# Kernel tuning notes

Hardware: AMD Instinct MI355X
Metric: run time of the kernel (lower is better)

## Reference

```python
import jax, jax.numpy as jnp
import numpy as np

B, S, D, H = 2, 2048, 768, 12
HD = D // H


def setup_inputs() -> dict:
    key = jax.random.key(0)
    ks = jax.random.split(key, 8)
    scale = 1.0 / np.sqrt(D)
    inp = {
        "q": jax.random.normal(ks[0], (B, S, D), jnp.float32),
        "k": jax.random.normal(ks[1], (B, S, D), jnp.float32),
        "v": jax.random.normal(ks[2], (B, S, D), jnp.float32),
        # causal mask: 1.0 where attention is disallowed (upper triangle)
        "mask": jnp.triu(jnp.ones((S, S), jnp.float32), k=1)[None, None, :, :],
        "Wq": jax.random.normal(ks[3], (D, D), jnp.float32) * scale,
        "bq": jnp.zeros((D,), jnp.float32),
        "Wk": jax.random.normal(ks[4], (D, D), jnp.float32) * scale,
        "bk": jnp.zeros((D,), jnp.float32),
        "Wv": jax.random.normal(ks[5], (D, D), jnp.float32) * scale,
        "bv": jnp.zeros((D,), jnp.float32),
        "Wo": jax.random.normal(ks[6], (D, D), jnp.float32) * scale,
        "bo": jnp.zeros((D,), jnp.float32),
    }
    return inp


def _split_heads(x):
    # [B, S, D] -> [B, H, S, HD]
    b, s, _ = x.shape
    return x.reshape(b, s, H, HD).transpose(0, 2, 1, 3)


def reference(q, k, v, mask, Wq, bq, Wk, bk, Wv, bv, Wo, bo):
    qh = _split_heads(q @ Wq + bq)
    kh = _split_heads(k @ Wk + bk)
    vh = _split_heads(v @ Wv + bv)
    scale = 1.0 / jnp.sqrt(jnp.asarray(HD, qh.dtype))
    # [B, H, Sq, Sk] — full attention matrix, as in the original
    scores = jnp.einsum("bhqd,bhkd->bhqk", qh, kh) * scale
    scores = scores + mask * -1e9
    attn = jax.nn.softmax(scores, axis=-1)  # dropout is identity at inference
    out = jnp.einsum("bhqk,bhkd->bhqd", attn, vh)
    out = out.transpose(0, 2, 1, 3).reshape(q.shape[0], -1, D)
    return out @ Wo + bo
```

## Files before the change

kernel.cpp:

```cpp
#include <hip/hip_runtime.h>

#define SEQ    2048
#define NB     2
#define DMODEL 768
#define NH     12
#define HDIM   64
#define BS     (NB * SEQ)

typedef __bf16  bf16x8  __attribute__((ext_vector_type(8)));
typedef ushort  ushort8 __attribute__((ext_vector_type(8)));
typedef float   floatx4 __attribute__((ext_vector_type(4)));

#define GLOBAL_AS __attribute__((address_space(1)))
#define LDS_AS    __attribute__((address_space(3)))

union PackU8 { ushort u[8]; uint4 v; };
union PackU4 { ushort u[4]; uint2 v; };

__device__ __forceinline__ ushort f2bf(float x) {
    union { float f; unsigned u; } t; t.f = x;
    unsigned r = t.u + 0x7fffu + ((t.u >> 16) & 1u);
    return (ushort)(r >> 16);
}

__device__ __forceinline__ bf16x8 ld_frag(const ushort* p) {
    return __builtin_bit_cast(bf16x8, *(const ushort8*)p);
}

__global__ void convert_x(const float* __restrict__ q, const float* __restrict__ k,
                          const float* __restrict__ v,
                          ushort* __restrict__ qo, ushort* __restrict__ ko,
                          ushort* __restrict__ vo)
{
    const float* src = blockIdx.z == 0 ? q : blockIdx.z == 1 ? k : v;
    ushort*      dst = blockIdx.z == 0 ? qo : blockIdx.z == 1 ? ko : vo;
    const int i = (blockIdx.x * 256 + threadIdx.x) * 4;
    const float4 f = *(const float4*)(src + i);
    ushort4 o;
    o.x = f2bf(f.x); o.y = f2bf(f.y); o.z = f2bf(f.z); o.w = f2bf(f.w);
    *(ushort4*)(dst + i) = o;
}

__global__ __launch_bounds__(256)
void convert_wT(const float* __restrict__ wq, const float* __restrict__ wk,
                const float* __restrict__ wv, const float* __restrict__ wo,
                ushort* __restrict__ wtcat, ushort* __restrict__ wto)
{
    __shared__ float Tf[64][69];
    const int z = blockIdx.z;
    const float* w = z == 0 ? wq : z == 1 ? wk : z == 2 ? wv : wo;
    ushort*      o = z < 3 ? wtcat + (size_t)z * DMODEL * DMODEL : wto;
    const int k0 = blockIdx.x * 64, n0 = blockIdx.y * 64;
    const int tid = threadIdx.x;
#pragma unroll
    for (int p = 0; p < 4; ++p) {
        const int idx = tid + p * 256;
        const int r = idx >> 4, c = (idx & 15) * 4;
        const float4 f = *(const float4*)&w[(size_t)(k0 + r) * DMODEL + n0 + c];
        Tf[r][c] = f.x; Tf[r][c + 1] = f.y; Tf[r][c + 2] = f.z; Tf[r][c + 3] = f.w;
    }
    __syncthreads();
#pragma unroll
    for (int p = 0; p < 2; ++p) {
        const int idx = tid + p * 256;
        const int n = idx >> 3, kk = (idx & 7) * 8;
        PackU8 pk;
#pragma unroll
        for (int j = 0; j < 8; ++j) pk.u[j] = f2bf(Tf[kk + j][n]);
        *(uint4*)&o[(size_t)(n0 + n) * DMODEL + k0 + kk] = pk.v;
    }
}

__global__ __launch_bounds__(256)
void gemm_qkv(const ushort* __restrict__ xq, const ushort* __restrict__ xk,
              const ushort* __restrict__ xv, const ushort* __restrict__ WT,
              const float* __restrict__ bq, const float* __restrict__ bk,
              const float* __restrict__ bv,
              ushort* __restrict__ oq, ushort* __restrict__ ok,
              ushort* __restrict__ ov)
{
    __shared__ __align__(16) ushort As[128 * 32];
    __shared__ __align__(16) ushort Bs[128 * 32];

    const int z = blockIdx.y / 6;
    const ushort* X = z == 0 ? xq : z == 1 ? xk : xv;

    const int tid  = threadIdx.x;
    const int lane = tid & 63;
    const int w    = tid >> 6;
    const int l15  = lane & 15;
    const int quad = lane >> 4;
    const int wm   = (w >> 1) * 64;
    const int wn   = (w & 1) * 64;
    const int row0 = blockIdx.x * 128;
    const int col0 = blockIdx.y * 128;

    floatx4 acc[4][4];
    const floatx4 fzero = {0.f, 0.f, 0.f, 0.f};
#pragma unroll
    for (int i = 0; i < 4; ++i)
#pragma unroll
        for (int j = 0; j < 4; ++j) acc[i][j] = fzero;

    const int rin = lane >> 2;
    const int gc  = (lane & 3) * 8;

    for (int k0 = 0; k0 < DMODEL; k0 += 32) {
#pragma unroll
        for (int p = 0; p < 2; ++p) {
            const int ch = w * 2 + p;
            const int r  = ch * 16 + rin;
            __builtin_amdgcn_global_load_lds(
                (const GLOBAL_AS uint*)&X[(size_t)(row0 + r) * DMODEL + k0 + gc],
                (LDS_AS uint*)&As[ch * 512], 16, 0, 0);
            __builtin_amdgcn_global_load_lds(
                (const GLOBAL_AS uint*)&WT[(size_t)(col0 + r) * DMODEL + k0 + gc],
                (LDS_AS uint*)&Bs[ch * 512], 16, 0, 0);
        }
        __syncthreads();

        bf16x8 af[4], bfr[4];
#pragma unroll
        for (int t = 0; t < 4; ++t) {
            af[t]  = ld_frag(&As[(wm + t * 16 + l15) * 32 + quad * 8]);
            bfr[t] = ld_frag(&Bs[(wn + t * 16 + l15) * 32 + quad * 8]);
        }
#pragma unroll
        for (int ti = 0; ti < 4; ++ti)
#pragma unroll
            for (int tj = 0; tj < 4; ++tj)
                acc[ti][tj] = __builtin_amdgcn_mfma_f32_16x16x32_bf16(
                    af[ti], bfr[tj], acc[ti][tj], 0, 0, 0);
        __syncthreads();
    }

    const int c0 = (blockIdx.y % 6) * 128;
    const float*  bias = z == 0 ? bq : z == 1 ? bk : bv;
    ushort*       out  = z == 0 ? oq : z == 1 ? ok : ov;
    const float   sc   = (z == 0) ? 0.18033688f : 1.f;
#pragma unroll
    for (int tj = 0; tj < 4; ++tj) {
        const int c_l = c0 + wn + tj * 16 + l15;
        const float bb = bias[c_l];
        const int h  = c_l >> 6;
        const int dd = c_l & 63;
#pragma unroll
        for (int ti = 0; ti < 4; ++ti) {
#pragma unroll
            for (int ri = 0; ri < 4; ++ri) {
                const int r_g = row0 + wm + ti * 16 + quad * 4 + ri;
                const int b   = r_g >> 11;
                const int s   = r_g & (SEQ - 1);
                out[(((size_t)(b * NH + h) * SEQ + s) << 6) + dd] =
                    f2bf((acc[ti][tj][ri] + bb) * sc);
            }
        }
    }
}

__global__ __launch_bounds__(256)
void gemm_out(const ushort* __restrict__ X, const ushort* __restrict__ WT,
              const float* __restrict__ bias, float* __restrict__ fo)
{
    __shared__ __align__(16) ushort As[64][40];
    __shared__ __align__(16) ushort Bs[128][40];

    const int tid  = threadIdx.x;
    const int lane = tid & 63;
    const int wv   = tid >> 6;
    const int wm   = (wv >> 1) * 32;
    const int wn   = (wv & 1) * 64;
    const int l15  = lane & 15;
    const int quad = lane >> 4;
    const int row0 = blockIdx.x * 64;
    const int col0 = blockIdx.y * 128;

    floatx4 acc[2][4];
    const floatx4 fzero = {0.f, 0.f, 0.f, 0.f};
#pragma unroll
    for (int i = 0; i < 2; ++i)
#pragma unroll
        for (int j = 0; j < 4; ++j) acc[i][j] = fzero;

    const int sr = tid >> 2;
    const int sc = (tid & 3) * 8;

    for (int k0 = 0; k0 < DMODEL; k0 += 32) {
        *(uint4*)&As[sr][sc] = *(const uint4*)&X[(size_t)(row0 + sr) * DMODEL + k0 + sc];
#pragma unroll
        for (int p = 0; p < 2; ++p) {
            const int r = sr + p * 64;
            *(uint4*)&Bs[r][sc] = *(const uint4*)&WT[(size_t)(col0 + r) * DMODEL + k0 + sc];
        }
        __syncthreads();

        bf16x8 af[2], bfr[4];
#pragma unroll
        for (int t = 0; t < 2; ++t)
            af[t] = ld_frag(&As[wm + t * 16 + l15][quad * 8]);
#pragma unroll
        for (int t = 0; t < 4; ++t)
            bfr[t] = ld_frag(&Bs[wn + t * 16 + l15][quad * 8]);
#pragma unroll
        for (int ti = 0; ti < 2; ++ti)
#pragma unroll
            for (int tj = 0; tj < 4; ++tj)
                acc[ti][tj] = __builtin_amdgcn_mfma_f32_16x16x32_bf16(
                    af[ti], bfr[tj], acc[ti][tj], 0, 0, 0);
        __syncthreads();
    }

#pragma unroll
    for (int tj = 0; tj < 4; ++tj) {
        const int c_g = col0 + wn + tj * 16 + l15;
        const float bb = bias[c_g];
#pragma unroll
        for (int ti = 0; ti < 2; ++ti)
#pragma unroll
            for (int ri = 0; ri < 4; ++ri) {
                const int r_g = row0 + wm + ti * 16 + quad * 4 + ri;
                fo[(size_t)r_g * DMODEL + c_g] = acc[ti][tj][ri] + bb;
            }
    }
}

__global__ void transpose_v(const ushort* __restrict__ vh, ushort* __restrict__ vt)
{
    __shared__ __align__(16) ushort T[64][72];
    const int bh = blockIdx.y;
    const int s0 = blockIdx.x * 64;
    const ushort* src = vh + (size_t)bh * SEQ * HDIM;
    ushort*       dst = vt + (size_t)bh * HDIM * SEQ;

#pragma unroll
    for (int p = 0; p < 2; ++p) {
        const int idx = threadIdx.x + p * 256;
        const int r = idx >> 3, c = (idx & 7) * 8;
        *(uint4*)&T[r][c] = *(const uint4*)&src[(size_t)(s0 + r) * HDIM + c];
    }
    __syncthreads();
#pragma unroll
    for (int p = 0; p < 2; ++p) {
        const int idx = threadIdx.x + p * 256;
        const int d = idx >> 3, c = (idx & 7) * 8;
        PackU8 pk;
#pragma unroll
        for (int j = 0; j < 8; ++j) pk.u[j] = T[c + j][d];
        *(uint4*)&dst[(size_t)d * SEQ + s0 + c] = pk.v;
    }
}

__global__ __launch_bounds__(64)
void attn_mfma(const ushort* __restrict__ qh, const ushort* __restrict__ kh,
               const ushort* __restrict__ vt, ushort* __restrict__ ctx)
{
    __shared__ __align__(16) ushort Ps[32][64];

    const int lane = threadIdx.x;
    const int l15  = lane & 15;
    const int quad = lane >> 4;
    const int e3   = l15 & 7;

    const int id  = blockIdx.x;
    const int xcd = id & 7;
    const int jj  = id >> 3;
    const int g   = jj >> 6;
    const int qt  = 63 - (jj & 63);
    const int bh  = xcd + 8 * g;
    const int b   = bh / NH, h = bh - b * NH;
    const int nk  = (qt >> 1) + 1;
    const size_t base = (size_t)bh * SEQ * HDIM;

    bf16x8 qf0[2], qf1[2];
#pragma unroll
    for (int ks = 0; ks < 2; ++ks) {
        qf0[ks] = ld_frag(&qh[base + (size_t)(qt * 32 +      l15) * HDIM + ks * 32 + quad * 8]);
        qf1[ks] = ld_frag(&qh[base + (size_t)(qt * 32 + 16 + l15) * HDIM + ks * 32 + quad * 8]);
    }

    float l0 = 0.f, l1 = 0.f;
    floatx4 O[4][2];
    const floatx4 fzero = {0.f, 0.f, 0.f, 0.f};
#pragma unroll
    for (int dj = 0; dj < 4; ++dj) { O[dj][0] = fzero; O[dj][1] = fzero; }

    const int rg0 = qt * 32 + l15;

    auto load_k = [&](bf16x8 (&kf)[4][2], int t) {
        const int c0 = t * 64;
#pragma unroll
        for (int nj = 0; nj < 4; ++nj)
#pragma unroll
            for (int ks = 0; ks < 2; ++ks)
                kf[nj][ks] = ld_frag(
                    &kh[base + (size_t)(c0 + nj * 16 + l15) * HDIM + ks * 32 + quad * 8]);
    };

    auto body = [&](const bf16x8 (&kf)[4][2], int t) {
        const int  c0   = t * 64;
        const bool diag = (t == nk - 1);

        bf16x8 vf[4][2];
#pragma unroll
        for (int dj = 0; dj < 4; ++dj)
#pragma unroll
            for (int ks = 0; ks < 2; ++ks)
                vf[dj][ks] = ld_frag(
                    &vt[base + (size_t)(dj * 16 + l15) * SEQ + c0 + ks * 32 + quad * 8]);

        floatx4 S[4][2];
        __builtin_amdgcn_s_setprio(1);
#pragma unroll
        for (int nj = 0; nj < 4; ++nj) {
            S[nj][0] = __builtin_amdgcn_mfma_f32_16x16x32_bf16(kf[nj][0], qf0[0], fzero, 0, 0, 0);
            S[nj][1] = __builtin_amdgcn_mfma_f32_16x16x32_bf16(kf[nj][0], qf1[0], fzero, 0, 0, 0);
            S[nj][0] = __builtin_amdgcn_mfma_f32_16x16x32_bf16(kf[nj][1], qf0[1], S[nj][0], 0, 0, 0);
            S[nj][1] = __builtin_amdgcn_mfma_f32_16x16x32_bf16(kf[nj][1], qf1[1], S[nj][1], 0, 0, 0);
        }
        __builtin_amdgcn_s_setprio(0);

        float rs0 = 0.f, rs1 = 0.f;
#pragma unroll
        for (int nj = 0; nj < 4; ++nj) {
            PackU4 p0, p1;
#pragma unroll
            for (int ri = 0; ri < 4; ++ri) {
                const int krow = c0 + nj * 16 + quad * 4 + ri;
                float v0 = __builtin_amdgcn_exp2f(S[nj][0][ri]);
                float v1 = __builtin_amdgcn_exp2f(S[nj][1][ri]);
                if (diag) {
                    if (krow > rg0)      v0 = 0.f;
                    if (krow > rg0 + 16) v1 = 0.f;
                }
                rs0 += v0; rs1 += v1;
                union { float f; unsigned u; } t0, t1;
                t0.f = v0; t1.f = v1;
                p0.u[ri] = (ushort)(t0.u >> 16);
                p1.u[ri] = (ushort)(t1.u >> 16);
            }
            *(uint2*)&Ps[l15     ][(nj * 16 + quad * 4) ^ (e3 << 3)] = p0.v;
            *(uint2*)&Ps[16 + l15][(nj * 16 + quad * 4) ^ (e3 << 3)] = p1.v;
        }
        rs0 += __shfl_xor(rs0, 16); rs0 += __shfl_xor(rs0, 32);
        rs1 += __shfl_xor(rs1, 16); rs1 += __shfl_xor(rs1, 32);
        l0 += rs0; l1 += rs1;

        bf16x8 pf0[2], pf1[2];
#pragma unroll
        for (int ks = 0; ks < 2; ++ks) {
            pf0[ks] = ld_frag(&Ps[l15     ][(ks * 32 + quad * 8) ^ (e3 << 3)]);
            pf1[ks] = ld_frag(&Ps[16 + l15][(ks * 32 + quad * 8) ^ (e3 << 3)]);
        }

        __builtin_amdgcn_s_setprio(1);
#pragma unroll
        for (int dj = 0; dj < 4; ++dj)
#pragma unroll
            for (int ks = 0; ks < 2; ++ks) {
                O[dj][0] = __builtin_amdgcn_mfma_f32_16x16x32_bf16(pf0[ks], vf[dj][ks], O[dj][0], 0, 0, 0);
                O[dj][1] = __builtin_amdgcn_mfma_f32_16x16x32_bf16(pf1[ks], vf[dj][ks], O[dj][1], 0, 0, 0);
            }
        __builtin_amdgcn_s_setprio(0);
    };

    bf16x8 kfA[4][2], kfB[4][2];
    load_k(kfA, 0);
    int t = 0;
    for (; t + 1 < nk; t += 2) {
        load_k(kfB, t + 1);
        body(kfA, t);
        if (t + 2 < nk) load_k(kfA, t + 2);
        body(kfB, t + 1);
    }
    if (t < nk) body(kfA, t);

    const float i0 = 1.f / l0, i1 = 1.f / l1;
    float ib0[4], ib1[4];
#pragma unroll
    for (int ri = 0; ri < 4; ++ri) {
        ib0[ri] = __shfl(i0, quad * 4 + ri);
        ib1[ri] = __shfl(i1, quad * 4 + ri);
    }
#pragma unroll
    for (int dj = 0; dj < 4; ++dj)
#pragma unroll
        for (int ri = 0; ri < 4; ++ri) {
            const int r0 = qt * 32 + quad * 4 + ri;
            ctx[((size_t)b * SEQ + r0) * DMODEL + h * HDIM + dj * 16 + l15] =
                f2bf(O[dj][0][ri] * ib0[ri]);
            ctx[((size_t)b * SEQ + r0 + 16) * DMODEL + h * HDIM + dj * 16 + l15] =
                f2bf(O[dj][1][ri] * ib1[ri]);
        }
}

extern "C" void kernel_launch(void* const* d_in, const int* in_sizes, int n_in,
                              void* d_out, int out_size, void* d_ws, size_t ws_size,
                              hipStream_t stream)
{
    const float* q  = (const float*)d_in[0];
    const float* k  = (const float*)d_in[1];
    const float* v  = (const float*)d_in[2];
    const float* Wq = (const float*)d_in[4];
    const float* bq = (const float*)d_in[5];
    const float* Wk = (const float*)d_in[6];
    const float* bk = (const float*)d_in[7];
    const float* Wv = (const float*)d_in[8];
    const float* bv = (const float*)d_in[9];
    const float* Wo = (const float*)d_in[10];
    const float* bo = (const float*)d_in[11];
    float* out = (float*)d_out;

    char* ws = (char*)d_ws;
    const size_t ACT = (size_t)BS * DMODEL * 2;
    ushort* qx    = (ushort*)(ws);
    ushort* kx    = (ushort*)(ws + ACT);
    ushort* vx    = (ushort*)(ws + 2 * ACT);
    ushort* qhp   = (ushort*)(ws + 3 * ACT);
    ushort* khp   = (ushort*)(ws + 4 * ACT);
    ushort* vhp   = (ushort*)(ws + 5 * ACT);
    ushort* wtcat = (ushort*)(ws + 6 * ACT);
    ushort* wto   = wtcat + (size_t)3 * DMODEL * DMODEL;
    ushort* vhT   = vx;
    ushort* ctx   = qx;

    convert_x<<<dim3(BS * DMODEL / 1024, 1, 3), 256, 0, stream>>>(q, k, v, qx, kx, vx);
    convert_wT<<<dim3(12, 12, 4), 256, 0, stream>>>(Wq, Wk, Wv, Wo, wtcat, wto);
    gemm_qkv<<<dim3(BS / 128, 18), 256, 0, stream>>>(
        qx, kx, vx, wtcat, bq, bk, bv, qhp, khp, vhp);
    transpose_v<<<dim3(SEQ / 64, NB * NH), 256, 0, stream>>>(vhp, vhT);
    attn_mfma<<<dim3(1536), 64, 0, stream>>>(qhp, khp, vhT, ctx);
    gemm_out<<<dim3(BS / 64, DMODEL / 128), 256, 0, stream>>>(ctx, wto, bo, out);
}
```

Baseline: 213.2 us.

## Split attention KV loop across four waves per block with LDS exchange

Runs the attention kernel with four waves per query tile. Each wave computes QK^T and exp for a different 64-key tile and writes the probabilities to its own LDS slot. After a barrier, every wave multiplies all four P tiles against its own 16-column slice of V. Row sums are combined through LDS at the end. This shortens each block's serial KV chain and lowers per-wave register use, at the cost of two barriers per step, dropping the K double-buffering, and redundant P reads from LDS.

```diff
diff --git a/kernel.cpp b/kernel.cpp
--- a/kernel.cpp
+++ b/kernel.cpp
@@ -250,13 +250,16 @@
     }
 }
 
-__global__ __launch_bounds__(64)
+__global__ __launch_bounds__(256, 4)
 void attn_mfma(const ushort* __restrict__ qh, const ushort* __restrict__ kh,
                const ushort* __restrict__ vt, ushort* __restrict__ ctx)
 {
-    __shared__ __align__(16) ushort Ps[32][64];
-
-    const int lane = threadIdx.x;
+    __shared__ __align__(16) ushort Ps[4][32][64];
+    __shared__ __align__(16) float  Lred[4][2][16];
+
+    const int tid  = threadIdx.x;
+    const int lane = tid & 63;
+    const int wv   = tid >> 6;
     const int l15  = lane & 15;
     const int quad = lane >> 4;
     const int e3   = l15 & 7;
@@ -279,118 +282,105 @@
     }
 
     float l0 = 0.f, l1 = 0.f;
-    floatx4 O[4][2];
+    floatx4 O0, O1;
     const floatx4 fzero = {0.f, 0.f, 0.f, 0.f};
-#pragma unroll
-    for (int dj = 0; dj < 4; ++dj) { O[dj][0] = fzero; O[dj][1] = fzero; }
+    O0 = fzero; O1 = fzero;
 
     const int rg0 = qt * 32 + l15;
 
-    auto load_k = [&](bf16x8 (&kf)[4][2], int t) {
-        const int c0 = t * 64;
-#pragma unroll
-        for (int nj = 0; nj < 4; ++nj)
-#pragma unroll
-            for (int ks = 0; ks < 2; ++ks)
-                kf[nj][ks] = ld_frag(
-                    &kh[base + (size_t)(c0 + nj * 16 + l15) * HDIM + ks * 32 + quad * 8]);
-    };
-
-    auto body = [&](const bf16x8 (&kf)[4][2], int t) {
-        const int  c0   = t * 64;
-        const bool diag = (t == nk - 1);
-
-        bf16x8 vf[4][2];
-#pragma unroll
-        for (int dj = 0; dj < 4; ++dj)
-#pragma unroll
-            for (int ks = 0; ks < 2; ++ks)
-                vf[dj][ks] = ld_frag(
-                    &vt[base + (size_t)(dj * 16 + l15) * SEQ + c0 + ks * 32 + quad * 8]);
-
-        floatx4 S[4][2];
-        __builtin_amdgcn_s_setprio(1);
-#pragma unroll
-        for (int nj = 0; nj < 4; ++nj) {
-            S[nj][0] = __builtin_amdgcn_mfma_f32_16x16x32_bf16(kf[nj][0], qf0[0], fzero, 0, 0, 0);
-            S[nj][1] = __builtin_amdgcn_mfma_f32_16x16x32_bf16(kf[nj][0], qf1[0], fzero, 0, 0, 0);
-            S[nj][0] = __builtin_amdgcn_mfma_f32_16x16x32_bf16(kf[nj][1], qf0[1], S[nj][0], 0, 0, 0);
-            S[nj][1] = __builtin_amdgcn_mfma_f32_16x16x32_bf16(kf[nj][1], qf1[1], S[nj][1], 0, 0, 0);
-        }
-        __builtin_amdgcn_s_setprio(0);
-
-        float rs0 = 0.f, rs1 = 0.f;
-#pragma unroll
-        for (int nj = 0; nj < 4; ++nj) {
-            PackU4 p0, p1;
-#pragma unroll
-            for (int ri = 0; ri < 4; ++ri) {
-                const int krow = c0 + nj * 16 + quad * 4 + ri;
-                float v0 = __builtin_amdgcn_exp2f(S[nj][0][ri]);
-                float v1 = __builtin_amdgcn_exp2f(S[nj][1][ri]);
-                if (diag) {
-                    if (krow > rg0)      v0 = 0.f;
-                    if (krow > rg0 + 16) v1 = 0.f;
+    for (int t4 = 0; t4 < nk; t4 += 4) {
+        const int kt = t4 + wv;
+
+        if (kt < nk) {
+            const int  c0   = kt * 64;
+            const bool diag = (kt == nk - 1);
+
+            bf16x8 kf[4][2];
+#pragma unroll
+            for (int nj = 0; nj < 4; ++nj)
+#pragma unroll
+                for (int ks = 0; ks < 2; ++ks)
+                    kf[nj][ks] = ld_frag(
+                        &kh[base + (size_t)(c0 + nj * 16 + l15) * HDIM + ks * 32 + quad * 8]);
+
+            float rs0 = 0.f, rs1 = 0.f;
+#pragma unroll
+            for (int nj = 0; nj < 4; ++nj) {
+                floatx4 s0, s1;
+                s0 = __builtin_amdgcn_mfma_f32_16x16x32_bf16(kf[nj][0], qf0[0], fzero, 0, 0, 0);
+                s1 = __builtin_amdgcn_mfma_f32_16x16x32_bf16(kf[nj][0], qf1[0], fzero, 0, 0, 0);
+                s0 = __builtin_amdgcn_mfma_f32_16x16x32_bf16(kf[nj][1], qf0[1], s0, 0, 0, 0);
+                s1 = __builtin_amdgcn_mfma_f32_16x16x32_bf16(kf[nj][1], qf1[1], s1, 0, 0, 0);
+
+                PackU4 p0, p1;
+#pragma unroll
+                for (int ri = 0; ri < 4; ++ri) {
+                    const int krow = c0 + nj * 16 + quad * 4 + ri;
+                    float v0 = __builtin_amdgcn_exp2f(s0[ri]);
+                    float v1 = __builtin_amdgcn_exp2f(s1[ri]);
+                    if (diag) {
+                        if (krow > rg0)      v0 = 0.f;
+                        if (krow > rg0 + 16) v1 = 0.f;
+                    }
+                    rs0 += v0; rs1 += v1;
+                    union { float f; unsigned u; } t0u, t1u;
+                    t0u.f = v0; t1u.f = v1;
+                    p0.u[ri] = (ushort)(t0u.u >> 16);
+                    p1.u[ri] = (ushort)(t1u.u >> 16);
                 }
-                rs0 += v0; rs1 += v1;
-                union { float f; unsigned u; } t0, t1;
-                t0.f = v0; t1.f = v1;
-                p0.u[ri] = (ushort)(t0.u >> 16);
-                p1.u[ri] = (ushort)(t1.u >> 16);
+                *(uint2*)&Ps[wv][l15     ][(nj * 16 + quad * 4) ^ (e3 << 3)] = p0.v;
+                *(uint2*)&Ps[wv][16 + l15][(nj * 16 + quad * 4) ^ (e3 << 3)] = p1.v;
             }
-            *(uint2*)&Ps[l15     ][(nj * 16 + quad * 4) ^ (e3 << 3)] = p0.v;
-            *(uint2*)&Ps[16 + l15][(nj * 16 + quad * 4) ^ (e3 << 3)] = p1.v;
-        }
-        rs0 += __shfl_xor(rs0, 16); rs0 += __shfl_xor(rs0, 32);
-        rs1 += __shfl_xor(rs1, 16); rs1 += __shfl_xor(rs1, 32);
-        l0 += rs0; l1 += rs1;
-
-        bf16x8 pf0[2], pf1[2];
-#pragma unroll
-        for (int ks = 0; ks < 2; ++ks) {
-            pf0[ks] = ld_frag(&Ps[l15     ][(ks * 32 + quad * 8) ^ (e3 << 3)]);
-            pf1[ks] = ld_frag(&Ps[16 + l15][(ks * 32 + quad * 8) ^ (e3 << 3)]);
-        }
-
-        __builtin_amdgcn_s_setprio(1);
-#pragma unroll
-        for (int dj = 0; dj < 4; ++dj)
-#pragma unroll
-            for (int ks = 0; ks < 2; ++ks) {
-                O[dj][0] = __builtin_amdgcn_mfma_f32_16x16x32_bf16(pf0[ks], vf[dj][ks], O[dj][0], 0, 0, 0);
-                O[dj][1] = __builtin_amdgcn_mfma_f32_16x16x32_bf16(pf1[ks], vf[dj][ks], O[dj][1], 0, 0, 0);
+            rs0 += __shfl_xor(rs0, 16); rs0 += __shfl_xor(rs0, 32);
+            rs1 += __shfl_xor(rs1, 16); rs1 += __shfl_xor(rs1, 32);
+            l0 += rs0; l1 += rs1;
+        }
+        __syncthreads();
+
+        const int na = (nk - t4 < 4) ? (nk - t4) : 4;
+#pragma unroll
+        for (int w = 0; w < 4; ++w) {
+            if (w < na) {
+                const int c0w = (t4 + w) * 64;
+                bf16x8 vf[2], pf0[2], pf1[2];
+#pragma unroll
+                for (int ks = 0; ks < 2; ++ks) {
+                    vf[ks]  = ld_frag(&vt[base + (size_t)(wv * 16 + l15) * SEQ + c0w + ks * 32 + quad * 8]);
+                    pf0[ks] = ld_frag(&Ps[w][l15     ][(ks * 32 + quad * 8) ^ (e3 << 3)]);
+                    pf1[ks] = ld_frag(&Ps[w][16 + l15][(ks * 32 + quad * 8) ^ (e3 << 3)]);
+                }
+#pragma unroll
+                for (int ks = 0; ks < 2; ++ks) {
+                    O0 = __builtin_amdgcn_mfma_f32_16x16x32_bf16(pf0[ks], vf[ks], O0, 0, 0, 0);
+                    O1 = __builtin_amdgcn_mfma_f32_16x16x32_bf16(pf1[ks], vf[ks], O1, 0, 0, 0);
+                }
             }
-        __builtin_amdgcn_s_setprio(0);
-    };
-
-    bf16x8 kfA[4][2], kfB[4][2];
-    load_k(kfA, 0);
-    int t = 0;
-    for (; t + 1 < nk; t += 2) {
-        load_k(kfB, t + 1);
-        body(kfA, t);
-        if (t + 2 < nk) load_k(kfA, t + 2);
-        body(kfB, t + 1);
-    }
-    if (t < nk) body(kfA, t);
-
-    const float i0 = 1.f / l0, i1 = 1.f / l1;
-    float ib0[4], ib1[4];
+        }
+        __syncthreads();
+    }
+
+    if (quad == 0) { Lred[wv][0][l15] = l0; Lred[wv][1][l15] = l1; }
+    __syncthreads();
+
+    float4 Ls0 = {0.f, 0.f, 0.f, 0.f}, Ls1 = {0.f, 0.f, 0.f, 0.f};
+#pragma unroll
+    for (int w = 0; w < 4; ++w) {
+        const float4 a = *(const float4*)&Lred[w][0][quad * 4];
+        const float4 c = *(const float4*)&Lred[w][1][quad * 4];
+        Ls0.x += a.x; Ls0.y += a.y; Ls0.z += a.z; Ls0.w += a.w;
+        Ls1.x += c.x; Ls1.y += c.y; Ls1.z += c.z; Ls1.w += c.w;
+    }
+    const float ib0[4] = {1.f / Ls0.x, 1.f / Ls0.y, 1.f / Ls0.z, 1.f / Ls0.w};
+    const float ib1[4] = {1.f / Ls1.x, 1.f / Ls1.y, 1.f / Ls1.z, 1.f / Ls1.w};
+
 #pragma unroll
     for (int ri = 0; ri < 4; ++ri) {
-        ib0[ri] = __shfl(i0, quad * 4 + ri);
-        ib1[ri] = __shfl(i1, quad * 4 + ri);
-    }
-#pragma unroll
-    for (int dj = 0; dj < 4; ++dj)
-#pragma unroll
-        for (int ri = 0; ri < 4; ++ri) {
-            const int r0 = qt * 32 + quad * 4 + ri;
-            ctx[((size_t)b * SEQ + r0) * DMODEL + h * HDIM + dj * 16 + l15] =
-                f2bf(O[dj][0][ri] * ib0[ri]);
-            ctx[((size_t)b * SEQ + r0 + 16) * DMODEL + h * HDIM + dj * 16 + l15] =
-                f2bf(O[dj][1][ri] * ib1[ri]);
-        }
+        const int r0 = qt * 32 + quad * 4 + ri;
+        ctx[((size_t)b * SEQ + r0) * DMODEL + h * HDIM + wv * 16 + l15] =
+            f2bf(O0[ri] * ib0[ri]);
+        ctx[((size_t)b * SEQ + r0 + 16) * DMODEL + h * HDIM + wv * 16 + l15] =
+            f2bf(O1[ri] * ib1[ri]);
+    }
 }
 
 extern "C" void kernel_launch(void* const* d_in, const int* in_sizes, int n_in,
@@ -428,6 +418,6 @@
     gemm_qkv<<<dim3(BS / 128, 18), 256, 0, stream>>>(
         qx, kx, vx, wtcat, bq, bk, bv, qhp, khp, vhp);
     transpose_v<<<dim3(SEQ / 64, NB * NH), 256, 0, stream>>>(vhp, vhT);
-    attn_mfma<<<dim3(1536), 64, 0, stream>>>(qhp, khp, vhT, ctx);
+    attn_mfma<<<dim3(1536), 256, 0, stream>>>(qhp, khp, vhT, ctx);
     gemm_out<<<dim3(BS / 64, DMODEL / 128), 256, 0, stream>>>(ctx, wto, bo, out);
 }
```

New measurement: 218.8 us. +2.6%, slower.

## Split attention block into two waves sharing double-buffered LDS K/V tiles

Applied to the files above, without the earlier changes.

The attention kernel now runs two waves per block, each owning 16 query rows instead of one wave owning 32. K and V tiles are staged into LDS with asynchronous global_load_lds into a swizzled double buffer and shared by both waves. The next tile's load is issued while the current tile is computed. This raises wave-level parallelism and removes duplicated global fragment loads, at the cost of a block barrier every tile and more LDS per block.

```diff
diff --git a/kernel.cpp b/kernel.cpp
--- a/kernel.cpp
+++ b/kernel.cpp
@@ -250,13 +250,17 @@
     }
 }
 
-__global__ __launch_bounds__(64)
+__global__ __launch_bounds__(128)
 void attn_mfma(const ushort* __restrict__ qh, const ushort* __restrict__ kh,
                const ushort* __restrict__ vt, ushort* __restrict__ ctx)
 {
+    __shared__ __align__(16) ushort Ks[2][64][64];
+    __shared__ __align__(16) ushort Vs[2][64][64];
     __shared__ __align__(16) ushort Ps[32][64];
 
-    const int lane = threadIdx.x;
+    const int tid  = threadIdx.x;
+    const int lane = tid & 63;
+    const int wv   = tid >> 6;
     const int l15  = lane & 15;
     const int quad = lane >> 4;
     const int e3   = l15 & 7;
@@ -271,125 +275,110 @@
     const int nk  = (qt >> 1) + 1;
     const size_t base = (size_t)bh * SEQ * HDIM;
 
-    bf16x8 qf0[2], qf1[2];
-#pragma unroll
-    for (int ks = 0; ks < 2; ++ks) {
-        qf0[ks] = ld_frag(&qh[base + (size_t)(qt * 32 +      l15) * HDIM + ks * 32 + quad * 8]);
-        qf1[ks] = ld_frag(&qh[base + (size_t)(qt * 32 + 16 + l15) * HDIM + ks * 32 + quad * 8]);
-    }
-
-    float l0 = 0.f, l1 = 0.f;
-    floatx4 O[4][2];
+    bf16x8 qf[2];
+#pragma unroll
+    for (int ks = 0; ks < 2; ++ks)
+        qf[ks] = ld_frag(&qh[base + (size_t)(qt * 32 + wv * 16 + l15) * HDIM + ks * 32 + quad * 8]);
+
+    const int srow = lane >> 3;
+    const int kcol = ((lane & 7) ^ (srow & 7)) * 8;
+
+    auto stage = [&](int bufi, int c0s) {
+#pragma unroll
+        for (int p = 0; p < 4; ++p) {
+            const int r = p * 16 + wv * 8 + srow;
+            __builtin_amdgcn_global_load_lds(
+                (const GLOBAL_AS uint*)&kh[base + (size_t)(c0s + r) * HDIM + kcol],
+                (LDS_AS uint*)&Ks[bufi][p * 16 + wv * 8][0], 16, 0, 0);
+            __builtin_amdgcn_global_load_lds(
+                (const GLOBAL_AS uint*)&vt[base + (size_t)r * SEQ + c0s + kcol],
+                (LDS_AS uint*)&Vs[bufi][p * 16 + wv * 8][0], 16, 0, 0);
+        }
+    };
+
+    stage(0, 0);
+
+    float l = 0.f;
+    floatx4 O[4];
     const floatx4 fzero = {0.f, 0.f, 0.f, 0.f};
 #pragma unroll
-    for (int dj = 0; dj < 4; ++dj) { O[dj][0] = fzero; O[dj][1] = fzero; }
-
-    const int rg0 = qt * 32 + l15;
-
-    auto load_k = [&](bf16x8 (&kf)[4][2], int t) {
-        const int c0 = t * 64;
-#pragma unroll
-        for (int nj = 0; nj < 4; ++nj)
-#pragma unroll
-            for (int ks = 0; ks < 2; ++ks)
-                kf[nj][ks] = ld_frag(
-                    &kh[base + (size_t)(c0 + nj * 16 + l15) * HDIM + ks * 32 + quad * 8]);
-    };
-
-    auto body = [&](const bf16x8 (&kf)[4][2], int t) {
+    for (int dj = 0; dj < 4; ++dj) O[dj] = fzero;
+
+    const int row_g = qt * 32 + wv * 16 + l15;
+
+    __syncthreads();
+
+    for (int t = 0; t < nk; ++t) {
+        const int  cur  = t & 1;
         const int  c0   = t * 64;
         const bool diag = (t == nk - 1);
 
-        bf16x8 vf[4][2];
-#pragma unroll
-        for (int dj = 0; dj < 4; ++dj)
-#pragma unroll
-            for (int ks = 0; ks < 2; ++ks)
-                vf[dj][ks] = ld_frag(
-                    &vt[base + (size_t)(dj * 16 + l15) * SEQ + c0 + ks * 32 + quad * 8]);
-
-        floatx4 S[4][2];
+        bf16x8 kf[4][2], vf[4][2];
+#pragma unroll
+        for (int nj = 0; nj < 4; ++nj)
+#pragma unroll
+            for (int ks = 0; ks < 2; ++ks) {
+                kf[nj][ks] = ld_frag(&Ks[cur][nj * 16 + l15][(ks * 32 + quad * 8) ^ (e3 << 3)]);
+                vf[nj][ks] = ld_frag(&Vs[cur][nj * 16 + l15][(ks * 32 + quad * 8) ^ (e3 << 3)]);
+            }
+
+        if (t + 1 < nk) stage(cur ^ 1, (t + 1) * 64);
+
+        floatx4 S[4];
         __builtin_amdgcn_s_setprio(1);
 #pragma unroll
         for (int nj = 0; nj < 4; ++nj) {
-            S[nj][0] = __builtin_amdgcn_mfma_f32_16x16x32_bf16(kf[nj][0], qf0[0], fzero, 0, 0, 0);
-            S[nj][1] = __builtin_amdgcn_mfma_f32_16x16x32_bf16(kf[nj][0], qf1[0], fzero, 0, 0, 0);
-            S[nj][0] = __builtin_amdgcn_mfma_f32_16x16x32_bf16(kf[nj][1], qf0[1], S[nj][0], 0, 0, 0);
-            S[nj][1] = __builtin_amdgcn_mfma_f32_16x16x32_bf16(kf[nj][1], qf1[1], S[nj][1], 0, 0, 0);
+            S[nj] = __builtin_amdgcn_mfma_f32_16x16x32_bf16(kf[nj][0], qf[0], fzero, 0, 0, 0);
+            S[nj] = __builtin_amdgcn_mfma_f32_16x16x32_bf16(kf[nj][1], qf[1], S[nj], 0, 0, 0);
         }
         __builtin_amdgcn_s_setprio(0);
 
-        float rs0 = 0.f, rs1 = 0.f;
+        float rs = 0.f;
 #pragma unroll
         for (int nj = 0; nj < 4; ++nj) {
-            PackU4 p0, p1;
+            PackU4 pk;
 #pragma unroll
             for (int ri = 0; ri < 4; ++ri) {
                 const int krow = c0 + nj * 16 + quad * 4 + ri;
-                float v0 = __builtin_amdgcn_exp2f(S[nj][0][ri]);
-                float v1 = __builtin_amdgcn_exp2f(S[nj][1][ri]);
-                if (diag) {
-                    if (krow > rg0)      v0 = 0.f;
-                    if (krow > rg0 + 16) v1 = 0.f;
-                }
-                rs0 += v0; rs1 += v1;
-                union { float f; unsigned u; } t0, t1;
-                t0.f = v0; t1.f = v1;
-                p0.u[ri] = (ushort)(t0.u >> 16);
-                p1.u[ri] = (ushort)(t1.u >> 16);
+                float p = __builtin_amdgcn_exp2f(S[nj][ri]);
+                if (diag && krow > row_g) p = 0.f;
+                rs += p;
+                union { float f; unsigned u; } tb; tb.f = p;
+                pk.u[ri] = (ushort)(tb.u >> 16);
             }
-            *(uint2*)&Ps[l15     ][(nj * 16 + quad * 4) ^ (e3 << 3)] = p0.v;
-            *(uint2*)&Ps[16 + l15][(nj * 16 + quad * 4) ^ (e3 << 3)] = p1.v;
-        }
-        rs0 += __shfl_xor(rs0, 16); rs0 += __shfl_xor(rs0, 32);
-        rs1 += __shfl_xor(rs1, 16); rs1 += __shfl_xor(rs1, 32);
-        l0 += rs0; l1 += rs1;
-
-        bf16x8 pf0[2], pf1[2];
-#pragma unroll
-        for (int ks = 0; ks < 2; ++ks) {
-            pf0[ks] = ld_frag(&Ps[l15     ][(ks * 32 + quad * 8) ^ (e3 << 3)]);
-            pf1[ks] = ld_frag(&Ps[16 + l15][(ks * 32 + quad * 8) ^ (e3 << 3)]);
-        }
+            *(uint2*)&Ps[wv * 16 + l15][(nj * 16 + quad * 4) ^ (e3 << 3)] = pk.v;
+        }
+        rs += __shfl_xor(rs, 16);
+        rs += __shfl_xor(rs, 32);
+        l += rs;
+
+        bf16x8 pf[2];
+#pragma unroll
+        for (int ks = 0; ks < 2; ++ks)
+            pf[ks] = ld_frag(&Ps[wv * 16 + l15][(ks * 32 + quad * 8) ^ (e3 << 3)]);
 
         __builtin_amdgcn_s_setprio(1);
 #pragma unroll
         for (int dj = 0; dj < 4; ++dj)
 #pragma unroll
-            for (int ks = 0; ks < 2; ++ks) {
-                O[dj][0] = __builtin_amdgcn_mfma_f32_16x16x32_bf16(pf0[ks], vf[dj][ks], O[dj][0], 0, 0, 0);
-                O[dj][1] = __builtin_amdgcn_mfma_f32_16x16x32_bf16(pf1[ks], vf[dj][ks], O[dj][1], 0, 0, 0);
-            }
+            for (int ks = 0; ks < 2; ++ks)
+                O[dj] = __builtin_amdgcn_mfma_f32_16x16x32_bf16(pf[ks], vf[dj][ks], O[dj], 0, 0, 0);
         __builtin_amdgcn_s_setprio(0);
-    };
-
-    bf16x8 kfA[4][2], kfB[4][2];
-    load_k(kfA, 0);
-    int t = 0;
-    for (; t + 1 < nk; t += 2) {
-        load_k(kfB, t + 1);
-        body(kfA, t);
-        if (t + 2 < nk) load_k(kfA, t + 2);
-        body(kfB, t + 1);
-    }
-    if (t < nk) body(kfA, t);
-
-    const float i0 = 1.f / l0, i1 = 1.f / l1;
-    float ib0[4], ib1[4];
-#pragma unroll
-    for (int ri = 0; ri < 4; ++ri) {
-        ib0[ri] = __shfl(i0, quad * 4 + ri);
-        ib1[ri] = __shfl(i1, quad * 4 + ri);
-    }
+
+        __syncthreads();
+    }
+
+    const float inv = 1.f / l;
+    float ib[4];
+#pragma unroll
+    for (int ri = 0; ri < 4; ++ri) ib[ri] = __shfl(inv, quad * 4 + ri);
 #pragma unroll
     for (int dj = 0; dj < 4; ++dj)
 #pragma unroll
         for (int ri = 0; ri < 4; ++ri) {
-            const int r0 = qt * 32 + quad * 4 + ri;
-            ctx[((size_t)b * SEQ + r0) * DMODEL + h * HDIM + dj * 16 + l15] =
-                f2bf(O[dj][0][ri] * ib0[ri]);
-            ctx[((size_t)b * SEQ + r0 + 16) * DMODEL + h * HDIM + dj * 16 + l15] =
-                f2bf(O[dj][1][ri] * ib1[ri]);
+            const int row = qt * 32 + wv * 16 + quad * 4 + ri;
+            ctx[((size_t)b * SEQ + row) * DMODEL + h * HDIM + dj * 16 + l15] =
+                f2bf(O[dj][ri] * ib[ri]);
         }
 }
 
@@ -428,6 +417,6 @@
     gemm_qkv<<<dim3(BS / 128, 18), 256, 0, stream>>>(
         qx, kx, vx, wtcat, bq, bk, bv, qhp, khp, vhp);
     transpose_v<<<dim3(SEQ / 64, NB * NH), 256, 0, stream>>>(vhp, vhT);
-    attn_mfma<<<dim3(1536), 64, 0, stream>>>(qhp, khp, vhT, ctx);
+    attn_mfma<<<dim3(1536), 128, 0, stream>>>(qhp, khp, vhT, ctx);
     gemm_out<<<dim3(BS / 64, DMODEL / 128), 256, 0, stream>>>(ctx, wto, bo, out);
 }
```

Result: faster. 200.6 us (-5.9%).

## Share K/V tiles across four waves via double-buffered LDS async loads

Applied to the files above, without the earlier changes.

The attention kernel moves from one 64-thread wave per 32-row query tile to four-wave blocks covering 128 query rows. K and V tiles are staged into double-buffered LDS with global_load_lds, so all four waves reuse each tile instead of each wave loading K/V fragments straight from global memory. This cuts redundant global/L2 traffic but adds barriers per step. Because of causality, some waves sit idle on the last tile while others still compute it. The grid shrinks from 1536 to 384 blocks, which lowers the number of concurrent work units.

```diff
diff --git a/kernel.cpp b/kernel.cpp
--- a/kernel.cpp
+++ b/kernel.cpp
@@ -250,13 +250,17 @@
     }
 }
 
-__global__ __launch_bounds__(64)
+__global__ __launch_bounds__(256, 3)
 void attn_mfma(const ushort* __restrict__ qh, const ushort* __restrict__ kh,
                const ushort* __restrict__ vt, ushort* __restrict__ ctx)
 {
-    __shared__ __align__(16) ushort Ps[32][64];
-
-    const int lane = threadIdx.x;
+    __shared__ __align__(16) ushort Ks[2][64][64];
+    __shared__ __align__(16) ushort Vs[2][64][64];
+    __shared__ __align__(16) ushort Ps[4][32][64];
+
+    const int tid  = threadIdx.x;
+    const int lane = tid & 63;
+    const int wv   = tid >> 6;
     const int l15  = lane & 15;
     const int quad = lane >> 4;
     const int e3   = l15 & 7;
@@ -264,19 +268,42 @@
     const int id  = blockIdx.x;
     const int xcd = id & 7;
     const int jj  = id >> 3;
-    const int g   = jj >> 6;
-    const int qt  = 63 - (jj & 63);
+    const int g   = jj >> 4;
+    const int qb  = 15 - (jj & 15);
     const int bh  = xcd + 8 * g;
     const int b   = bh / NH, h = bh - b * NH;
-    const int nk  = (qt >> 1) + 1;
+    const int nk  = 2 * qb + 2;
     const size_t base = (size_t)bh * SEQ * HDIM;
 
+    const int R   = qb * 128 + wv * 32;
+    const int t_d = R >> 6;
+
     bf16x8 qf0[2], qf1[2];
 #pragma unroll
     for (int ks = 0; ks < 2; ++ks) {
-        qf0[ks] = ld_frag(&qh[base + (size_t)(qt * 32 +      l15) * HDIM + ks * 32 + quad * 8]);
-        qf1[ks] = ld_frag(&qh[base + (size_t)(qt * 32 + 16 + l15) * HDIM + ks * 32 + quad * 8]);
-    }
+        qf0[ks] = ld_frag(&qh[base + (size_t)(R +      l15) * HDIM + ks * 32 + quad * 8]);
+        qf1[ks] = ld_frag(&qh[base + (size_t)(R + 16 + l15) * HDIM + ks * 32 + quad * 8]);
+    }
+    asm volatile("s_waitcnt vmcnt(0)" ::: "memory");
+
+    const int srow = lane >> 3;
+    const int kcol = ((lane & 7) ^ srow) * 8;
+
+    auto stage = [&](int bufi, int c0s) {
+#pragma unroll
+        for (int p = 0; p < 2; ++p) {
+            const int r = wv * 16 + p * 8 + srow;
+            __builtin_amdgcn_global_load_lds(
+                (const GLOBAL_AS uint*)&kh[base + (size_t)(c0s + r) * HDIM + kcol],
+                (LDS_AS uint*)&Ks[bufi][wv * 16 + p * 8][0], 16, 0, 0);
+            __builtin_amdgcn_global_load_lds(
+                (const GLOBAL_AS uint*)&vt[base + (size_t)r * SEQ + c0s + kcol],
+                (LDS_AS uint*)&Vs[bufi][wv * 16 + p * 8][0], 16, 0, 0);
+        }
+    };
+
+    stage(0, 0);
+    stage(1, 64);
 
     float l0 = 0.f, l1 = 0.f;
     floatx4 O[4][2];
@@ -284,95 +311,90 @@
 #pragma unroll
     for (int dj = 0; dj < 4; ++dj) { O[dj][0] = fzero; O[dj][1] = fzero; }
 
-    const int rg0 = qt * 32 + l15;
-
-    auto load_k = [&](bf16x8 (&kf)[4][2], int t) {
-        const int c0 = t * 64;
-#pragma unroll
-        for (int nj = 0; nj < 4; ++nj)
-#pragma unroll
-            for (int ks = 0; ks < 2; ++ks)
-                kf[nj][ks] = ld_frag(
-                    &kh[base + (size_t)(c0 + nj * 16 + l15) * HDIM + ks * 32 + quad * 8]);
-    };
-
-    auto body = [&](const bf16x8 (&kf)[4][2], int t) {
-        const int  c0   = t * 64;
-        const bool diag = (t == nk - 1);
-
-        bf16x8 vf[4][2];
-#pragma unroll
-        for (int dj = 0; dj < 4; ++dj)
-#pragma unroll
-            for (int ks = 0; ks < 2; ++ks)
-                vf[dj][ks] = ld_frag(
-                    &vt[base + (size_t)(dj * 16 + l15) * SEQ + c0 + ks * 32 + quad * 8]);
-
-        floatx4 S[4][2];
-        __builtin_amdgcn_s_setprio(1);
-#pragma unroll
-        for (int nj = 0; nj < 4; ++nj) {
-            S[nj][0] = __builtin_amdgcn_mfma_f32_16x16x32_bf16(kf[nj][0], qf0[0], fzero, 0, 0, 0);
-            S[nj][1] = __builtin_amdgcn_mfma_f32_16x16x32_bf16(kf[nj][0], qf1[0], fzero, 0, 0, 0);
-            S[nj][0] = __builtin_amdgcn_mfma_f32_16x16x32_bf16(kf[nj][1], qf0[1], S[nj][0], 0, 0, 0);
-            S[nj][1] = __builtin_amdgcn_mfma_f32_16x16x32_bf16(kf[nj][1], qf1[1], S[nj][1], 0, 0, 0);
-        }
-        __builtin_amdgcn_s_setprio(0);
-
-        float rs0 = 0.f, rs1 = 0.f;
-#pragma unroll
-        for (int nj = 0; nj < 4; ++nj) {
-            PackU4 p0, p1;
-#pragma unroll
-            for (int ri = 0; ri < 4; ++ri) {
-                const int krow = c0 + nj * 16 + quad * 4 + ri;
-                float v0 = __builtin_amdgcn_exp2f(S[nj][0][ri]);
-                float v1 = __builtin_amdgcn_exp2f(S[nj][1][ri]);
-                if (diag) {
-                    if (krow > rg0)      v0 = 0.f;
-                    if (krow > rg0 + 16) v1 = 0.f;
+    for (int t = 0; t < nk; ++t) {
+        const int  cur = t & 1;
+        const int  c0  = t * 64;
+
+        if (t + 1 < nk) asm volatile("s_waitcnt vmcnt(4)" ::: "memory");
+        else            asm volatile("s_waitcnt vmcnt(0)" ::: "memory");
+        __builtin_amdgcn_s_barrier();
+
+        const bool act = (t <= t_d);
+
+        bf16x8 kf[4][2], vf[4][2];
+        if (act) {
+#pragma unroll
+            for (int nj = 0; nj < 4; ++nj)
+#pragma unroll
+                for (int ks = 0; ks < 2; ++ks) {
+                    kf[nj][ks] = ld_frag(&Ks[cur][nj * 16 + l15][(ks * 32 + quad * 8) ^ (e3 << 3)]);
+                    vf[nj][ks] = ld_frag(&Vs[cur][nj * 16 + l15][(ks * 32 + quad * 8) ^ (e3 << 3)]);
                 }
-                rs0 += v0; rs1 += v1;
-                union { float f; unsigned u; } t0, t1;
-                t0.f = v0; t1.f = v1;
-                p0.u[ri] = (ushort)(t0.u >> 16);
-                p1.u[ri] = (ushort)(t1.u >> 16);
+        }
+
+        asm volatile("s_waitcnt lgkmcnt(0)" ::: "memory");
+        __builtin_amdgcn_s_barrier();
+        if (t + 2 < nk) stage(cur, (t + 2) * 64);
+
+        if (act) {
+            const bool diag = (t == t_d);
+
+            floatx4 S[4][2];
+            __builtin_amdgcn_s_setprio(1);
+#pragma unroll
+            for (int nj = 0; nj < 4; ++nj) {
+                S[nj][0] = __builtin_amdgcn_mfma_f32_16x16x32_bf16(kf[nj][0], qf0[0], fzero, 0, 0, 0);
+                S[nj][1] = __builtin_amdgcn_mfma_f32_16x16x32_bf16(kf[nj][0], qf1[0], fzero, 0, 0, 0);
+                S[nj][0] = __builtin_amdgcn_mfma_f32_16x16x32_bf16(kf[nj][1], qf0[1], S[nj][0], 0, 0, 0);
+                S[nj][1] = __builtin_amdgcn_mfma_f32_16x16x32_bf16(kf[nj][1], qf1[1], S[nj][1], 0, 0, 0);
             }
-            *(uint2*)&Ps[l15     ][(nj * 16 + quad * 4) ^ (e3 << 3)] = p0.v;
-            *(uint2*)&Ps[16 + l15][(nj * 16 + quad * 4) ^ (e3 << 3)] = p1.v;
-        }
-        rs0 += __shfl_xor(rs0, 16); rs0 += __shfl_xor(rs0, 32);
-        rs1 += __shfl_xor(rs1, 16); rs1 += __shfl_xor(rs1, 32);
-        l0 += rs0; l1 += rs1;
-
-        bf16x8 pf0[2], pf1[2];
-#pragma unroll
-        for (int ks = 0; ks < 2; ++ks) {
-            pf0[ks] = ld_frag(&Ps[l15     ][(ks * 32 + quad * 8) ^ (e3 << 3)]);
-            pf1[ks] = ld_frag(&Ps[16 + l15][(ks * 32 + quad * 8) ^ (e3 << 3)]);
-        }
-
-        __builtin_amdgcn_s_setprio(1);
-#pragma unroll
-        for (int dj = 0; dj < 4; ++dj)
+            __builtin_amdgcn_s_setprio(0);
+
+            float rs0 = 0.f, rs1 = 0.f;
+            const int rg0 = R + l15;
+#pragma unroll
+            for (int nj = 0; nj < 4; ++nj) {
+                PackU4 p0, p1;
+#pragma unroll
+                for (int ri = 0; ri < 4; ++ri) {
+                    const int krow = c0 + nj * 16 + quad * 4 + ri;
+                    float v0 = __builtin_amdgcn_exp2f(S[nj][0][ri]);
+                    float v1 = __builtin_amdgcn_exp2f(S[nj][1][ri]);
+                    if (diag) {
+                        if (krow > rg0)      v0 = 0.f;
+                        if (krow > rg0 + 16) v1 = 0.f;
+                    }
+                    rs0 += v0; rs1 += v1;
+                    union { float f; unsigned u; } t0u, t1u;
+                    t0u.f = v0; t1u.f = v1;
+                    p0.u[ri] = (ushort)(t0u.u >> 16);
+                    p1.u[ri] = (ushort)(t1u.u >> 16);
+                }
+                *(uint2*)&Ps[wv][l15     ][(nj * 16 + quad * 4) ^ (e3 << 3)] = p0.v;
+                *(uint2*)&Ps[wv][16 + l15][(nj * 16 + quad * 4) ^ (e3 << 3)] = p1.v;
+            }
+            rs0 += __shfl_xor(rs0, 16); rs0 += __shfl_xor(rs0, 32);
+            rs1 += __shfl_xor(rs1, 16); rs1 += __shfl_xor(rs1, 32);
+            l0 += rs0; l1 += rs1;
+
+            bf16x8 pf0[2], pf1[2];
 #pragma unroll
             for (int ks = 0; ks < 2; ++ks) {
-                O[dj][0] = __builtin_amdgcn_mfma_f32_16x16x32_bf16(pf0[ks], vf[dj][ks], O[dj][0], 0, 0, 0);
-                O[dj][1] = __builtin_amdgcn_mfma_f32_16x16x32_bf16(pf1[ks], vf[dj][ks], O[dj][1], 0, 0, 0);
+                pf0[ks] = ld_frag(&Ps[wv][l15     ][(ks * 32 + quad * 8) ^ (e3 << 3)]);
+                pf1[ks] = ld_frag(&Ps[wv][16 + l15][(ks * 32 + quad * 8) ^ (e3 << 3)]);
             }
-        __builtin_amdgcn_s_setprio(0);
-    };
-
-    bf16x8 kfA[4][2], kfB[4][2];
-    load_k(kfA, 0);
-    int t = 0;
-    for (; t + 1 < nk; t += 2) {
-        load_k(kfB, t + 1);
-        body(kfA, t);
-        if (t + 2 < nk) load_k(kfA, t + 2);
-        body(kfB, t + 1);
-    }
-    if (t < nk) body(kfA, t);
+
+            __builtin_amdgcn_s_setprio(1);
+#pragma unroll
+            for (int dj = 0; dj < 4; ++dj)
+#pragma unroll
+                for (int ks = 0; ks < 2; ++ks) {
+                    O[dj][0] = __builtin_amdgcn_mfma_f32_16x16x32_bf16(pf0[ks], vf[dj][ks], O[dj][0], 0, 0, 0);
+                    O[dj][1] = __builtin_amdgcn_mfma_f32_16x16x32_bf16(pf1[ks], vf[dj][ks], O[dj][1], 0, 0, 0);
+                }
+            __builtin_amdgcn_s_setprio(0);
+        }
+    }
 
     const float i0 = 1.f / l0, i1 = 1.f / l1;
     float ib0[4], ib1[4];
@@ -385,7 +407,7 @@
     for (int dj = 0; dj < 4; ++dj)
 #pragma unroll
         for (int ri = 0; ri < 4; ++ri) {
-            const int r0 = qt * 32 + quad * 4 + ri;
+            const int r0 = R + quad * 4 + ri;
             ctx[((size_t)b * SEQ + r0) * DMODEL + h * HDIM + dj * 16 + l15] =
                 f2bf(O[dj][0][ri] * ib0[ri]);
             ctx[((size_t)b * SEQ + r0 + 16) * DMODEL + h * HDIM + dj * 16 + l15] =
@@ -428,6 +450,6 @@
     gemm_qkv<<<dim3(BS / 128, 18), 256, 0, stream>>>(
         qx, kx, vx, wtcat, bq, bk, bv, qhp, khp, vhp);
     transpose_v<<<dim3(SEQ / 64, NB * NH), 256, 0, stream>>>(vhp, vhT);
-    attn_mfma<<<dim3(1536), 64, 0, stream>>>(qhp, khp, vhT, ctx);
+    attn_mfma<<<dim3(384), 256, 0, stream>>>(qhp, khp, vhT, ctx);
     gemm_out<<<dim3(BS / 64, DMODEL / 128), 256, 0, stream>>>(ctx, wto, bo, out);
 }
```

Result: slower. 265.7 us (+24.6%).
